# Kernel optimization log

Hardware: AMD Instinct MI355X
Metric: run time of the kernel (lower is better)

Reference implementation:

```python
import jax, jax.numpy as jnp
import numpy as np

N, FIN, F, H = 4096, 128, 64, 8
NEG = -1e10


def setup_inputs() -> dict:
    key = jax.random.key(0)
    ks = jax.random.split(key, 6)
    X = jax.random.normal(ks[0], (N, FIN), dtype=jnp.float32)
    # sparse-ish binary adjacency with self loops, stored dense (as the layer expects)
    A = (jax.random.uniform(ks[1], (N, N)) < 0.05).astype(jnp.int32)
    A = A.at[jnp.arange(N), jnp.arange(N)].set(1)
    W = jax.random.normal(ks[2], (H, FIN, F), dtype=jnp.float32) * (1.0 / np.sqrt(FIN))
    b = jnp.zeros((H, F), dtype=jnp.float32)
    a_self = jax.random.normal(ks[3], (H, F), dtype=jnp.float32) * (1.0 / np.sqrt(F))
    a_neigh = jax.random.normal(ks[4], (H, F), dtype=jnp.float32) * (1.0 / np.sqrt(F))
    return {"X": X, "A": A, "W": W, "b": b, "a_self": a_self, "a_neigh": a_neigh}


def reference(X, A, W, b, a_self, a_neigh):
    # Dropout layers run in inference mode in the original call -> identity.
    feats = jnp.einsum('nf,hfo->hno', X, W)              # [H, N, F]
    s_self = jnp.einsum('hno,ho->hn', feats, a_self)     # [H, N]
    s_neigh = jnp.einsum('hno,ho->hn', feats, a_neigh)   # [H, N]
    scores = s_self[:, :, None] + s_neigh[:, None, :]    # [H, N, N]
    scores = jnp.where(scores > 0, scores, 0.2 * scores)  # LeakyReLU(0.2)
    mask = (1.0 - A.astype(jnp.float32)) * NEG            # [N, N]
    attn = jax.nn.softmax(scores + mask[None], axis=-1)   # [H, N, N]
    out = jnp.einsum('hnm,hmo->hno', attn, feats) + b[:, None, :]
    out = jax.nn.elu(out)                                 # [H, N, F]
    # concat heads -> [N, H*F]
    return jnp.transpose(out, (1, 0, 2)).reshape(N, H * F)
```

## Files before the change

### kernel.cpp

```cpp
#include <hip/hip_runtime.h>
#include <cmath>


#define NN 4096
#define FIN 128
#define FF 64
#define HH 8

typedef _Float16 h2 __attribute__((ext_vector_type(2)));
typedef _Float16 h4 __attribute__((ext_vector_type(4)));
typedef _Float16 h8 __attribute__((ext_vector_type(8)));
typedef float f32x2 __attribute__((ext_vector_type(2)));
typedef float f32x4 __attribute__((ext_vector_type(4)));

union H8 {
  h8 v;
  h2 p[4];
};
union H4 {
  h4 v;
  h2 p[2];
};

static __device__ __forceinline__ float dot2acc(h2 a, float c) {
#if __has_builtin(__builtin_amdgcn_fdot2)
  return __builtin_amdgcn_fdot2(a, (h2){(_Float16)1.f, (_Float16)1.f}, c,
                                false);
#else
  return c + (float)a[0] + (float)a[1];
#endif
}

__global__ __launch_bounds__(256) void pack_kernel(
    const int* __restrict__ A, const float* __restrict__ W,
    const float* __restrict__ X, unsigned long long* __restrict__ bits,
    _Float16* __restrict__ Wsw, _Float16* __restrict__ Xsw) {
  const int b = blockIdx.x;
  const int tid = threadIdx.x;
  const int wave = tid >> 6, lane = tid & 63;
  if (b < NN) {
    __shared__ int ldsT[4][4][256];
    const int* ar = A + (size_t)b * NN;
    int4 v[4];
#pragma unroll
    for (int it = 0; it < 4; ++it) {
      const int g = wave * 4 + it;
      v[it] = *(const int4*)(ar + g * 256 + lane * 4);
    }
#pragma unroll
    for (int it = 0; it < 4; ++it) *(int4*)&ldsT[wave][it][lane * 4] = v[it];
    unsigned long long* br = bits + ((size_t)b << 6);
#pragma unroll
    for (int it = 0; it < 4; ++it) {
      const int g = wave * 4 + it;
      int w0 = ldsT[wave][it][0 * 64 + lane];
      int w1 = ldsT[wave][it][1 * 64 + lane];
      int w2 = ldsT[wave][it][2 * 64 + lane];
      int w3 = ldsT[wave][it][3 * 64 + lane];
      unsigned long long m0 = __ballot(w0 != 0);
      unsigned long long m1 = __ballot(w1 != 0);
      unsigned long long m2 = __ballot(w2 != 0);
      unsigned long long m3 = __ballot(w3 != 0);
      if (lane == 0) {
        ulonglong2 p0 = {m0, m1}, p1 = {m2, m3};
        *(ulonglong2*)(br + g * 4 + 0) = p0;
        *(ulonglong2*)(br + g * 4 + 2) = p1;
      }
    }
  } else if (b < NN + 2) {
    const int h0 = (b - NN) * 4;
    for (int h = h0; h < h0 + 4; ++h) {
      for (int c = tid; c < 1024; c += 256) {
        int ln = c & 63, nb = (c >> 6) & 3, kt = c >> 8;
        int f = nb * 16 + (ln & 15);
        int k0 = kt * 32 + (ln >> 4) * 8;
        h8 v;
#pragma unroll
        for (int j = 0; j < 8; ++j)
          v[j] = (_Float16)W[((size_t)(h * FIN) + k0 + j) * FF + f];
        *(h8*)(Wsw + ((size_t)(((h * 4 + kt) * 4 + nb) * 64 + ln)) * 8) = v;
      }
    }
  } else {
    const int tile = (b - NN - 2) * 4 + wave;
    const int l16 = lane & 15, quad = lane >> 4;
    const float* xr = X + (size_t)(tile * 16 + l16) * FIN;
#pragma unroll
    for (int kt = 0; kt < 4; ++kt) {
      int k0 = kt * 32 + quad * 8;
      f32x4 x0 = *(const f32x4*)(xr + k0);
      f32x4 x1 = *(const f32x4*)(xr + k0 + 4);
      h8 v = {(_Float16)x0[0], (_Float16)x0[1], (_Float16)x0[2],
              (_Float16)x0[3], (_Float16)x1[0], (_Float16)x1[1],
              (_Float16)x1[2], (_Float16)x1[3]};
      *(h8*)(Xsw + ((size_t)((tile * 4 + kt) * 64 + lane)) * 8) = v;
    }
  }
}

__global__ __launch_bounds__(256) void feats_kernel(
    const _Float16* __restrict__ Xsw, const _Float16* __restrict__ Wsw,
    const float* __restrict__ a_self, const float* __restrict__ a_neigh,
    _Float16* __restrict__ feats_sw, _Float16* __restrict__ es_h,
    _Float16* __restrict__ esn_h, _Float16* __restrict__ et_h,
    _Float16* __restrict__ etn_h) {
  const int h = blockIdx.y;
  const int tid = threadIdx.x, wave = tid >> 6, lane = tid & 63;
  const int l16 = lane & 15, quad = lane >> 4;
  const int rt = blockIdx.x * 4 + wave;
  const int r0 = rt * 16;

  f32x4 acc[4];
#pragma unroll
  for (int nb = 0; nb < 4; ++nb) acc[nb] = (f32x4){0.f, 0.f, 0.f, 0.f};

  const _Float16* xp = Xsw + ((size_t)(rt * 4) * 64 + lane) * 8;
  const _Float16* wp = Wsw + ((size_t)(h * 16) * 64 + lane) * 8;
  h8 Af[4];
#pragma unroll
  for (int kt = 0; kt < 4; ++kt) Af[kt] = *(const h8*)(xp + kt * 512);
#pragma unroll
  for (int kt = 0; kt < 4; ++kt)
#pragma unroll
    for (int nb = 0; nb < 4; ++nb) {
      h8 Bf = *(const h8*)(wp + (kt * 4 + nb) * 512);
      acc[nb] = __builtin_amdgcn_mfma_f32_16x16x32_f16(Af[kt], Bf, acc[nb], 0, 0, 0);
    }

  float as[4], an[4];
#pragma unroll
  for (int nb = 0; nb < 4; ++nb) {
    as[nb] = a_self[h * FF + nb * 16 + l16];
    an[nb] = a_neigh[h * FF + nb * 16 + l16];
  }
#pragma unroll
  for (int r = 0; r < 4; ++r) {
    float ps = acc[0][r] * as[0] + acc[1][r] * as[1] + acc[2][r] * as[2] +
               acc[3][r] * as[3];
    float pn = acc[0][r] * an[0] + acc[1][r] * an[1] + acc[2][r] * an[2] +
               acc[3][r] * an[3];
#pragma unroll
    for (int m = 1; m <= 8; m <<= 1) {
      ps += __shfl_xor(ps, m, 64);
      pn += __shfl_xor(pn, m, 64);
    }
    if (l16 == 0) {
      int node = h * NN + r0 + quad * 4 + r;
      es_h[node] = (_Float16)__expf(ps - 2.0f);
      esn_h[node] = (_Float16)__expf(0.2f * ps - 2.0f);
      et_h[node] = (_Float16)__expf(pn - 2.0f);
      etn_h[node] = (_Float16)__expf(0.2f * pn - 2.0f);
    }
  }

  const int kb = r0 >> 5;
  const int quadA = ((r0 >> 4) & 1) * 2 + (quad >> 1);
  const int jbase = (quad & 1) << 2;
#pragma unroll
  for (int nb = 0; nb < 4; ++nb) {
    h4 v = {(_Float16)acc[nb][0], (_Float16)acc[nb][1], (_Float16)acc[nb][2],
            (_Float16)acc[nb][3]};
    size_t off = ((size_t)((h * 128 + kb) * 4 + nb) << 9) +
                 ((quadA * 16 + l16) << 3) + jbase;
    *(h4*)(feats_sw + off) = v;
  }
}

__global__ __launch_bounds__(512, 4) void attn_kernel(
    const unsigned long long* __restrict__ Abits,
    const _Float16* __restrict__ feats_sw, const _Float16* __restrict__ es_h,
    const _Float16* __restrict__ esn_h, const _Float16* __restrict__ et_h,
    const _Float16* __restrict__ etn_h, const float* __restrict__ bias,
    float* __restrict__ out) {
  const int bid = blockIdx.x;
  const int h = bid & 7, n0 = (bid >> 3) << 6;
  const int tid = threadIdx.x, wave = tid >> 6, lane = tid & 63;
  const int l16 = lane & 15, quad = lane >> 4;

  __shared__ h4 lut16[16];
  __shared__ float accL[8][16][66];
  __shared__ float denL[8][64];
  if (tid < 16) {
    h4 m;
#pragma unroll
    for (int j = 0; j < 4; ++j) m[j] = (_Float16)((tid >> j) & 1);
    lut16[tid] = m;
  }
  __syncthreads();

  h2 esp[4], esnp[4];
#pragma unroll
  for (int rg = 0; rg < 4; ++rg) {
    _Float16 e = es_h[h * NN + n0 + rg * 16 + l16];
    _Float16 en = esn_h[h * NN + n0 + rg * 16 + l16];
    esp[rg] = (h2){e, e};
    esnp[rg] = (h2){en, en};
  }

  f32x4 acc[4][4];
  float dsA[4] = {0.f, 0.f, 0.f, 0.f}, dsB[4] = {0.f, 0.f, 0.f, 0.f};
#pragma unroll
  for (int rg = 0; rg < 4; ++rg)
#pragma unroll
    for (int nb = 0; nb < 4; ++nb) acc[rg][nb] = (f32x4){0.f, 0.f, 0.f, 0.f};

  const uint2* ab = (const uint2*)Abits;
  const int rowbase = n0 + l16;
  const _Float16* etp = et_h + h * NN + (quad << 3);
  const _Float16* etnp = etn_h + h * NN + (quad << 3);
  const _Float16* fb = feats_sw + ((size_t)h << 18) + (lane << 3);

  for (int ct = wave; ct < 64; ct += 8) {
    uint2 bits[4];
#pragma unroll
    for (int rg = 0; rg < 4; ++rg)
      bits[rg] = ab[((rowbase + rg * 16) << 6) + ct];
    const _Float16* fbt = fb + (ct << 12);
#pragma unroll
    for (int kf = 0; kf < 2; ++kf) {
      H8 ET, ETN;
      ET.v = *(const h8*)(etp + (ct << 6) + kf * 32);
      ETN.v = *(const h8*)(etnp + (ct << 6) + kf * 32);
      const _Float16* fk = fbt + (kf << 11);
      h8 B0 = *(const h8*)(fk);
      h8 B1 = *(const h8*)(fk + 512);
      h8 B2 = *(const h8*)(fk + 1024);
      h8 B3 = *(const h8*)(fk + 1536);
#pragma unroll
      for (int rg = 0; rg < 4; ++rg) {
        unsigned word = kf ? bits[rg].y : bits[rg].x;
        unsigned byt = (word >> (quad << 3)) & 0xFFu;
        H4 mlo, mhi;
        mlo.v = lut16[byt & 15u];
        mhi.v = lut16[byt >> 4];
        H8 P;
#pragma unroll
        for (int p = 0; p < 4; ++p) {
          h2 a = esp[rg] * ET.p[p];
          h2 b = esnp[rg] * ETN.p[p];
          h2 r = __builtin_elementwise_max(a, b);
          h2 pm = r * (p < 2 ? mlo.p[p] : mhi.p[p - 2]);
          P.p[p] = pm;
          if (p & 1)
            dsB[rg] = dot2acc(pm, dsB[rg]);
          else
            dsA[rg] = dot2acc(pm, dsA[rg]);
        }
        acc[rg][0] =
            __builtin_amdgcn_mfma_f32_16x16x32_f16(P.v, B0, acc[rg][0], 0, 0, 0);
        acc[rg][1] =
            __builtin_amdgcn_mfma_f32_16x16x32_f16(P.v, B1, acc[rg][1], 0, 0, 0);
        acc[rg][2] =
            __builtin_amdgcn_mfma_f32_16x16x32_f16(P.v, B2, acc[rg][2], 0, 0, 0);
        acc[rg][3] =
            __builtin_amdgcn_mfma_f32_16x16x32_f16(P.v, B3, acc[rg][3], 0, 0, 0);
      }
    }
  }

#pragma unroll
  for (int rg = 0; rg < 4; ++rg) {
    float d = dsA[rg] + dsB[rg];
    d += __shfl_xor(d, 16, 64);
    d += __shfl_xor(d, 32, 64);
    if (quad == 0) denL[wave][rg * 16 + l16] = d;
  }

  const int erow = tid >> 5, ec0 = (tid & 31) << 1;
#pragma unroll
  for (int ph = 0; ph < 4; ++ph) {
    __syncthreads();
#pragma unroll
    for (int nb = 0; nb < 4; ++nb)
#pragma unroll
      for (int r = 0; r < 4; ++r)
        accL[wave][quad * 4 + r][nb * 16 + l16] = acc[ph][nb][r];
    __syncthreads();
    const int grow = ph * 16 + erow;
    float dn = 0.f;
#pragma unroll
    for (int w = 0; w < 8; ++w) dn += denL[w][grow];
    float inv = 1.0f / dn;
    f32x2 v = (f32x2){0.f, 0.f};
#pragma unroll
    for (int w = 0; w < 8; ++w) v += *(const f32x2*)&accL[w][erow][ec0];
    const f32x2 bv = *(const f32x2*)(bias + h * FF + ec0);
#pragma unroll
    for (int i = 0; i < 2; ++i) {
      float x = v[i] * inv + bv[i];
      v[i] = x > 0.f ? x : (__expf(x) - 1.0f);
    }
    *(f32x2*)(out + (size_t)(n0 + grow) * (HH * FF) + h * FF + ec0) = v;
  }
}

extern "C" void kernel_launch(void* const* d_in, const int* in_sizes, int n_in,
                              void* d_out, int out_size, void* d_ws,
                              size_t ws_size, hipStream_t stream) {
  const float* X = (const float*)d_in[0];
  const int* A = (const int*)d_in[1];
  const float* W = (const float*)d_in[2];
  const float* b = (const float*)d_in[3];
  const float* a_self = (const float*)d_in[4];
  const float* a_neigh = (const float*)d_in[5];
  float* out = (float*)d_out;

  char* ws = (char*)d_ws;
  unsigned long long* Abits = (unsigned long long*)ws;
  _Float16* feats_sw = (_Float16*)(ws + (2u << 20));
  _Float16* es_h = (_Float16*)(ws + (6u << 20));
  _Float16* esn_h = (_Float16*)(ws + (6u << 20) + (64u << 10));
  _Float16* et_h = (_Float16*)(ws + (6u << 20) + (128u << 10));
  _Float16* etn_h = (_Float16*)(ws + (6u << 20) + (192u << 10));
  _Float16* Wsw = (_Float16*)(ws + (6u << 20) + (256u << 10));
  _Float16* Xsw = (_Float16*)(ws + (6u << 20) + (384u << 10));

  pack_kernel<<<NN + 66, 256, 0, stream>>>(A, W, X, Abits, Wsw, Xsw);
  feats_kernel<<<dim3(64, 8), 256, 0, stream>>>(Xsw, Wsw, a_self, a_neigh,
                                                feats_sw, es_h, esn_h, et_h,
                                                etn_h);
  attn_kernel<<<512, 512, 0, stream>>>(Abits, feats_sw, es_h, esn_h, et_h,
                                       etn_h, b, out);
}
```

Measured before the change: 148.3 us.

## Halve attention block size and software-pipeline adjacency and feature loads

The attention kernel now runs 256 threads (4 waves) per block instead of 512, so each wave covers 16 column tiles instead of 8. The main loop is software-pipelined: the next tile's adjacency bits, feature fragments and exponent vectors are prefetched into registers while the current half-tile's MFMAs run. The epilogue reduction is adjusted to 4 waves and uses 16-byte stores. This aims to hide global-load latency behind compute, at the cost of more register pressure and fewer waves per block to hide latency.

```diff
diff --git a/kernel.cpp b/kernel.cpp
--- a/kernel.cpp
+++ b/kernel.cpp
@@ -166,7 +166,7 @@
   }
 }
 
-__global__ __launch_bounds__(512, 4) void attn_kernel(
+__global__ __launch_bounds__(256, 3) void attn_kernel(
     const unsigned long long* __restrict__ Abits,
     const _Float16* __restrict__ feats_sw, const _Float16* __restrict__ es_h,
     const _Float16* __restrict__ esn_h, const _Float16* __restrict__ et_h,
@@ -178,8 +178,8 @@
   const int l16 = lane & 15, quad = lane >> 4;
 
   __shared__ h4 lut16[16];
-  __shared__ float accL[8][16][66];
-  __shared__ float denL[8][64];
+  __shared__ float accL[4][16][66];
+  __shared__ float denL[4][64];
   if (tid < 16) {
     h4 m;
 #pragma unroll
@@ -205,58 +205,101 @@
     for (int nb = 0; nb < 4; ++nb) acc[rg][nb] = (f32x4){0.f, 0.f, 0.f, 0.f};
 
   const uint2* ab = (const uint2*)Abits;
-  const int rowbase = n0 + l16;
+  int bOff[4];
+#pragma unroll
+  for (int rg = 0; rg < 4; ++rg) bOff[rg] = (n0 + rg * 16 + l16) << 6;
   const _Float16* etp = et_h + h * NN + (quad << 3);
   const _Float16* etnp = etn_h + h * NN + (quad << 3);
   const _Float16* fb = feats_sw + ((size_t)h << 18) + (lane << 3);
 
-  for (int ct = wave; ct < 64; ct += 8) {
-    uint2 bits[4];
-#pragma unroll
-    for (int rg = 0; rg < 4; ++rg)
-      bits[rg] = ab[((rowbase + rg * 16) << 6) + ct];
-    const _Float16* fbt = fb + (ct << 12);
-#pragma unroll
-    for (int kf = 0; kf < 2; ++kf) {
-      H8 ET, ETN;
-      ET.v = *(const h8*)(etp + (ct << 6) + kf * 32);
-      ETN.v = *(const h8*)(etnp + (ct << 6) + kf * 32);
-      const _Float16* fk = fbt + (kf << 11);
-      h8 B0 = *(const h8*)(fk);
-      h8 B1 = *(const h8*)(fk + 512);
-      h8 B2 = *(const h8*)(fk + 1024);
-      h8 B3 = *(const h8*)(fk + 1536);
-#pragma unroll
-      for (int rg = 0; rg < 4; ++rg) {
-        unsigned word = kf ? bits[rg].y : bits[rg].x;
-        unsigned byt = (word >> (quad << 3)) & 0xFFu;
-        H4 mlo, mhi;
-        mlo.v = lut16[byt & 15u];
-        mhi.v = lut16[byt >> 4];
-        H8 P;
-#pragma unroll
-        for (int p = 0; p < 4; ++p) {
-          h2 a = esp[rg] * ET.p[p];
-          h2 b = esnp[rg] * ETN.p[p];
-          h2 r = __builtin_elementwise_max(a, b);
-          h2 pm = r * (p < 2 ? mlo.p[p] : mhi.p[p - 2]);
-          P.p[p] = pm;
-          if (p & 1)
-            dsB[rg] = dot2acc(pm, dsB[rg]);
-          else
-            dsA[rg] = dot2acc(pm, dsA[rg]);
-        }
-        acc[rg][0] =
-            __builtin_amdgcn_mfma_f32_16x16x32_f16(P.v, B0, acc[rg][0], 0, 0, 0);
-        acc[rg][1] =
-            __builtin_amdgcn_mfma_f32_16x16x32_f16(P.v, B1, acc[rg][1], 0, 0, 0);
-        acc[rg][2] =
-            __builtin_amdgcn_mfma_f32_16x16x32_f16(P.v, B2, acc[rg][2], 0, 0, 0);
-        acc[rg][3] =
-            __builtin_amdgcn_mfma_f32_16x16x32_f16(P.v, B3, acc[rg][3], 0, 0, 0);
-      }
-    }
-  }
+#define COMPUTE_KF(w0_, w1_, w2_, w3_, Bq0, Bq1, Bq2, Bq3, ETu, ETNu)         \
+  do {                                                                        \
+    const unsigned wl_[4] = {w0_, w1_, w2_, w3_};                             \
+    _Pragma("unroll") for (int rg = 0; rg < 4; ++rg) {                        \
+      const unsigned byt_ = (wl_[rg] >> (quad << 3)) & 0xFFu;                 \
+      H4 mlo_, mhi_;                                                          \
+      mlo_.v = lut16[byt_ & 15u];                                             \
+      mhi_.v = lut16[byt_ >> 4];                                              \
+      H8 P_;                                                                  \
+      _Pragma("unroll") for (int p = 0; p < 4; ++p) {                         \
+        h2 a_ = esp[rg] * ETu.p[p];                                           \
+        h2 b_ = esnp[rg] * ETNu.p[p];                                         \
+        h2 r_ = __builtin_elementwise_max(a_, b_);                            \
+        h2 pm_ = r_ * (p < 2 ? mlo_.p[p] : mhi_.p[p - 2]);                    \
+        P_.p[p] = pm_;                                                        \
+        if (p & 1)                                                            \
+          dsB[rg] = dot2acc(pm_, dsB[rg]);                                    \
+        else                                                                  \
+          dsA[rg] = dot2acc(pm_, dsA[rg]);                                    \
+      }                                                                       \
+      acc[rg][0] = __builtin_amdgcn_mfma_f32_16x16x32_f16(P_.v, Bq0,          \
+                                                          acc[rg][0], 0, 0,   \
+                                                          0);                 \
+      acc[rg][1] = __builtin_amdgcn_mfma_f32_16x16x32_f16(P_.v, Bq1,          \
+                                                          acc[rg][1], 0, 0,   \
+                                                          0);                 \
+      acc[rg][2] = __builtin_amdgcn_mfma_f32_16x16x32_f16(P_.v, Bq2,          \
+                                                          acc[rg][2], 0, 0,   \
+                                                          0);                 \
+      acc[rg][3] = __builtin_amdgcn_mfma_f32_16x16x32_f16(P_.v, Bq3,          \
+                                                          acc[rg][3], 0, 0,   \
+                                                          0);                 \
+    }                                                                         \
+  } while (0)
+
+  int ct = wave;
+  uint2 bitsC[4], bitsN[4];
+#pragma unroll
+  for (int rg = 0; rg < 4; ++rg) bitsC[rg] = ab[bOff[rg] + ct];
+  H8 ET0, ET1, ETN0, ETN1;
+  ET0.v = *(const h8*)(etp + (ct << 6));
+  ET1.v = *(const h8*)(etp + (ct << 6) + 32);
+  ETN0.v = *(const h8*)(etnp + (ct << 6));
+  ETN1.v = *(const h8*)(etnp + (ct << 6) + 32);
+  h8 BA0, BA1, BA2, BA3, BB0, BB1, BB2, BB3;
+  {
+    const _Float16* f0 = fb + ((size_t)ct << 12);
+    BA0 = *(const h8*)(f0);
+    BA1 = *(const h8*)(f0 + 512);
+    BA2 = *(const h8*)(f0 + 1024);
+    BA3 = *(const h8*)(f0 + 1536);
+  }
+
+  for (int it = 0; it < 16; ++it) {
+    const int ctn = (ct + 4) & 63;
+    {
+      const _Float16* f1 = fb + ((size_t)ct << 12) + 2048;
+      BB0 = *(const h8*)(f1);
+      BB1 = *(const h8*)(f1 + 512);
+      BB2 = *(const h8*)(f1 + 1024);
+      BB3 = *(const h8*)(f1 + 1536);
+    }
+#pragma unroll
+    for (int rg = 0; rg < 4; ++rg) bitsN[rg] = ab[bOff[rg] + ctn];
+
+    COMPUTE_KF(bitsC[0].x, bitsC[1].x, bitsC[2].x, bitsC[3].x, BA0, BA1, BA2,
+               BA3, ET0, ETN0);
+
+    ET0.v = *(const h8*)(etp + (ctn << 6));
+    ETN0.v = *(const h8*)(etnp + (ctn << 6));
+    {
+      const _Float16* f0n = fb + ((size_t)ctn << 12);
+      BA0 = *(const h8*)(f0n);
+      BA1 = *(const h8*)(f0n + 512);
+      BA2 = *(const h8*)(f0n + 1024);
+      BA3 = *(const h8*)(f0n + 1536);
+    }
+
+    COMPUTE_KF(bitsC[0].y, bitsC[1].y, bitsC[2].y, bitsC[3].y, BB0, BB1, BB2,
+               BB3, ET1, ETN1);
+
+    ET1.v = *(const h8*)(etp + (ctn << 6) + 32);
+    ETN1.v = *(const h8*)(etnp + (ctn << 6) + 32);
+#pragma unroll
+    for (int rg = 0; rg < 4; ++rg) bitsC[rg] = bitsN[rg];
+    ct = ctn;
+  }
+#undef COMPUTE_KF
 
 #pragma unroll
   for (int rg = 0; rg < 4; ++rg) {
@@ -266,7 +309,7 @@
     if (quad == 0) denL[wave][rg * 16 + l16] = d;
   }
 
-  const int erow = tid >> 5, ec0 = (tid & 31) << 1;
+  const int erow = tid >> 4, ec0 = (tid & 15) << 2;
 #pragma unroll
   for (int ph = 0; ph < 4; ++ph) {
     __syncthreads();
@@ -277,20 +320,26 @@
         accL[wave][quad * 4 + r][nb * 16 + l16] = acc[ph][nb][r];
     __syncthreads();
     const int grow = ph * 16 + erow;
-    float dn = 0.f;
-#pragma unroll
-    for (int w = 0; w < 8; ++w) dn += denL[w][grow];
+    float dn = denL[0][grow] + denL[1][grow] + denL[2][grow] + denL[3][grow];
     float inv = 1.0f / dn;
-    f32x2 v = (f32x2){0.f, 0.f};
-#pragma unroll
-    for (int w = 0; w < 8; ++w) v += *(const f32x2*)&accL[w][erow][ec0];
-    const f32x2 bv = *(const f32x2*)(bias + h * FF + ec0);
-#pragma unroll
-    for (int i = 0; i < 2; ++i) {
-      float x = v[i] * inv + bv[i];
-      v[i] = x > 0.f ? x : (__expf(x) - 1.0f);
-    }
-    *(f32x2*)(out + (size_t)(n0 + grow) * (HH * FF) + h * FF + ec0) = v;
+    f32x2 v0 = (f32x2){0.f, 0.f}, v1 = (f32x2){0.f, 0.f};
+#pragma unroll
+    for (int w = 0; w < 4; ++w) {
+      v0 += *(const f32x2*)&accL[w][erow][ec0];
+      v1 += *(const f32x2*)&accL[w][erow][ec0 + 2];
+    }
+    const f32x4 bv = *(const f32x4*)(bias + h * FF + ec0);
+    f32x4 o;
+    o[0] = v0[0];
+    o[1] = v0[1];
+    o[2] = v1[0];
+    o[3] = v1[1];
+#pragma unroll
+    for (int i = 0; i < 4; ++i) {
+      float x = o[i] * inv + bv[i];
+      o[i] = x > 0.f ? x : (__expf(x) - 1.0f);
+    }
+    *(f32x4*)(out + (size_t)(n0 + grow) * (HH * FF) + h * FF + ec0) = o;
   }
 }
 
@@ -319,6 +368,6 @@
   feats_kernel<<<dim3(64, 8), 256, 0, stream>>>(Xsw, Wsw, a_self, a_neigh,
                                                 feats_sw, es_h, esn_h, et_h,
                                                 etn_h);
-  attn_kernel<<<512, 512, 0, stream>>>(Abits, feats_sw, es_h, esn_h, et_h,
+  attn_kernel<<<512, 256, 0, stream>>>(Abits, feats_sw, es_h, esn_h, et_h,
                                        etn_h, b, out);
 }
```

After: 150.9 us. No clear change (+1.7%).

## Restructure attention kernel with LDS triple-buffered async staging and per-wave row split

Applied to the files above, without the earlier changes.

The attention kernel now gives each block 128 rows. Each wave owns 16 rows and walks all key columns, instead of splitting columns across waves and reducing the partial sums through LDS. Feature, et and mask-bit tiles are staged into a three-deep LDS ring with global_load_lds and explicit vmcnt waits. This overlaps memory traffic with the MFMA work and removes the cross-wave accumulator reduction. The LUT-based mask expansion is replaced by a bitfield-extract and perm AND mask. In exchange, the grid has half as many blocks and occupancy is lower, and the hand-written waitcnt counts are fragile.

```diff
diff --git a/kernel.cpp b/kernel.cpp
--- a/kernel.cpp
+++ b/kernel.cpp
@@ -17,9 +17,9 @@
   h8 v;
   h2 p[4];
 };
-union H4 {
-  h4 v;
-  h2 p[2];
+union U2 {
+  h2 h;
+  unsigned u;
 };
 
 static __device__ __forceinline__ float dot2acc(h2 a, float c) {
@@ -29,6 +29,24 @@
 #else
   return c + (float)a[0] + (float)a[1];
 #endif
+}
+
+static __device__ __forceinline__ unsigned mask2(unsigned w, int j) {
+#if __has_builtin(__builtin_amdgcn_sbfe) && __has_builtin(__builtin_amdgcn_perm)
+  int lo = __builtin_amdgcn_sbfe((int)w, j, 1);
+  int hi = __builtin_amdgcn_sbfe((int)w, j + 1, 1);
+  return __builtin_amdgcn_perm((unsigned)hi, (unsigned)lo, 0x05040100u);
+#else
+  int lo = ((int)(w << (31 - j))) >> 31;
+  int hi = ((int)(w << (30 - j))) >> 31;
+  return ((unsigned)lo & 0xFFFFu) | ((unsigned)hi << 16);
+#endif
+}
+
+static __device__ __forceinline__ void gload16(const void* g, void* l) {
+  __builtin_amdgcn_global_load_lds(
+      (const __attribute__((address_space(1))) unsigned int*)g,
+      (__attribute__((address_space(3))) unsigned int*)l, 16, 0, 0);
 }
 
 __global__ __launch_bounds__(256) void pack_kernel(
@@ -166,131 +184,133 @@
   }
 }
 
-__global__ __launch_bounds__(512, 4) void attn_kernel(
+__global__ __launch_bounds__(512, 2) void attn_kernel(
     const unsigned long long* __restrict__ Abits,
     const _Float16* __restrict__ feats_sw, const _Float16* __restrict__ es_h,
     const _Float16* __restrict__ esn_h, const _Float16* __restrict__ et_h,
     const _Float16* __restrict__ etn_h, const float* __restrict__ bias,
     float* __restrict__ out) {
   const int bid = blockIdx.x;
-  const int h = bid & 7, n0 = (bid >> 3) << 6;
+  const int h = bid & 7, n0 = (bid >> 3) << 7;
   const int tid = threadIdx.x, wave = tid >> 6, lane = tid & 63;
   const int l16 = lane & 15, quad = lane >> 4;
-
-  __shared__ h4 lut16[16];
-  __shared__ float accL[8][16][66];
-  __shared__ float denL[8][64];
-  if (tid < 16) {
-    h4 m;
-#pragma unroll
-    for (int j = 0; j < 4; ++j) m[j] = (_Float16)((tid >> j) & 1);
-    lut16[tid] = m;
-  }
-  __syncthreads();
-
-  h2 esp[4], esnp[4];
-#pragma unroll
-  for (int rg = 0; rg < 4; ++rg) {
-    _Float16 e = es_h[h * NN + n0 + rg * 16 + l16];
-    _Float16 en = esn_h[h * NN + n0 + rg * 16 + l16];
-    esp[rg] = (h2){e, e};
-    esnp[rg] = (h2){en, en};
-  }
-
-  f32x4 acc[4][4];
-  float dsA[4] = {0.f, 0.f, 0.f, 0.f}, dsB[4] = {0.f, 0.f, 0.f, 0.f};
-#pragma unroll
-  for (int rg = 0; rg < 4; ++rg)
-#pragma unroll
-    for (int nb = 0; nb < 4; ++nb) acc[rg][nb] = (f32x4){0.f, 0.f, 0.f, 0.f};
-
-  const uint2* ab = (const uint2*)Abits;
-  const int rowbase = n0 + l16;
-  const _Float16* etp = et_h + h * NN + (quad << 3);
-  const _Float16* etnp = etn_h + h * NN + (quad << 3);
-  const _Float16* fb = feats_sw + ((size_t)h << 18) + (lane << 3);
-
-  for (int ct = wave; ct < 64; ct += 8) {
-    uint2 bits[4];
-#pragma unroll
-    for (int rg = 0; rg < 4; ++rg)
-      bits[rg] = ab[((rowbase + rg * 16) << 6) + ct];
-    const _Float16* fbt = fb + (ct << 12);
-#pragma unroll
-    for (int kf = 0; kf < 2; ++kf) {
-      H8 ET, ETN;
-      ET.v = *(const h8*)(etp + (ct << 6) + kf * 32);
-      ETN.v = *(const h8*)(etnp + (ct << 6) + kf * 32);
-      const _Float16* fk = fbt + (kf << 11);
-      h8 B0 = *(const h8*)(fk);
-      h8 B1 = *(const h8*)(fk + 512);
-      h8 B2 = *(const h8*)(fk + 1024);
-      h8 B3 = *(const h8*)(fk + 1536);
-#pragma unroll
-      for (int rg = 0; rg < 4; ++rg) {
-        unsigned word = kf ? bits[rg].y : bits[rg].x;
-        unsigned byt = (word >> (quad << 3)) & 0xFFu;
-        H4 mlo, mhi;
-        mlo.v = lut16[byt & 15u];
-        mhi.v = lut16[byt >> 4];
+  const int shq = quad << 3;
+
+  __shared__ __align__(16) char smem[3 * 20480];
+
+  const int myrow = n0 + (wave << 4) + l16;
+  _Float16 e = es_h[h * NN + myrow];
+  _Float16 en = esn_h[h * NN + myrow];
+  const h2 esp = (h2){e, e};
+  const h2 esnp = (h2){en, en};
+
+  f32x4 acc[4];
+#pragma unroll
+  for (int nb = 0; nb < 4; ++nb) acc[nb] = (f32x4){0.f, 0.f, 0.f, 0.f};
+  float dsA = 0.f, dsB = 0.f;
+
+  const char* gF = (const char*)feats_sw + ((size_t)h << 19);
+  const char* gE = (const char*)et_h + (h << 13);
+  const char* gEN = (const char*)etn_h + (h << 13);
+  const char* gB = (const char*)Abits + ((size_t)n0 << 9);
+
+#define STAGE(s_, bw_)                                                        \
+  do {                                                                        \
+    char* L_ = smem + (bw_)*20480;                                            \
+    const char* src_ = gF + ((size_t)(s_) << 14) + (wave << 11) + (lane << 4);\
+    gload16(src_, L_ + (wave << 11) + (lane << 4));                           \
+    gload16(src_ + 1024, L_ + (wave << 11) + 1024 + (lane << 4));             \
+    if (wave == 0)                                                            \
+      gload16(gE + ((s_) << 8) + (l16 << 4), L_ + 16384 + (lane << 4));       \
+    if (wave == 1)                                                            \
+      gload16(gEN + ((s_) << 8) + (l16 << 4), L_ + 17408 + (lane << 4));      \
+    if (wave == 2)                                                            \
+      gload16(gB + ((size_t)lane << 9) + ((s_) << 4),                         \
+              L_ + 18432 + (lane << 4));                                      \
+    if (wave == 3)                                                            \
+      gload16(gB + ((size_t)(64 + lane) << 9) + ((s_) << 4),                  \
+              L_ + 18432 + 1024 + (lane << 4));                               \
+  } while (0)
+
+  STAGE(0, 0);
+  STAGE(1, 1);
+
+  for (int s = 0; s < 32; ++s) {
+    const int bC = s % 3;
+    if (s < 30) {
+      STAGE(s + 2, (s + 2) % 3);
+      __builtin_amdgcn_sched_barrier(0);
+      if (wave < 4)
+        asm volatile("s_waitcnt vmcnt(6)" ::: "memory");
+      else
+        asm volatile("s_waitcnt vmcnt(4)" ::: "memory");
+    } else if (s == 30) {
+      __builtin_amdgcn_sched_barrier(0);
+      if (wave < 4)
+        asm volatile("s_waitcnt vmcnt(3)" ::: "memory");
+      else
+        asm volatile("s_waitcnt vmcnt(2)" ::: "memory");
+    } else {
+      __builtin_amdgcn_sched_barrier(0);
+      asm volatile("s_waitcnt vmcnt(0)" ::: "memory");
+    }
+    __builtin_amdgcn_sched_barrier(0);
+    __builtin_amdgcn_s_barrier();
+
+    const char* L = smem + bC * 20480;
+#pragma unroll
+    for (int c = 0; c < 2; ++c) {
+      unsigned long long myb = *(const unsigned long long*)(
+          L + 18432 + (((wave << 4) + l16) << 4) + (c << 3));
+#pragma unroll
+      for (int kf = 0; kf < 2; ++kf) {
+        H8 ET, ETN;
+        ET.v = *(const h8*)(L + 16384 + (c << 7) + (kf << 6) + (quad << 4));
+        ETN.v = *(const h8*)(L + 17408 + (c << 7) + (kf << 6) + (quad << 4));
+        const char* fB = L + (c << 13) + (kf << 12) + (lane << 4);
+        h8 B0 = *(const h8*)(fB);
+        h8 B1 = *(const h8*)(fB + 1024);
+        h8 B2 = *(const h8*)(fB + 2048);
+        h8 B3 = *(const h8*)(fB + 3072);
+        unsigned wsw = (unsigned)(myb >> (kf ? 32 : 0)) >> shq;
         H8 P;
 #pragma unroll
         for (int p = 0; p < 4; ++p) {
-          h2 a = esp[rg] * ET.p[p];
-          h2 b = esnp[rg] * ETN.p[p];
-          h2 r = __builtin_elementwise_max(a, b);
-          h2 pm = r * (p < 2 ? mlo.p[p] : mhi.p[p - 2]);
-          P.p[p] = pm;
+          h2 a_ = esp * ET.p[p];
+          h2 b_ = esnp * ETN.p[p];
+          h2 r_ = __builtin_elementwise_max(a_, b_);
+          U2 u_;
+          u_.h = r_;
+          u_.u &= mask2(wsw, 2 * p);
+          P.p[p] = u_.h;
           if (p & 1)
-            dsB[rg] = dot2acc(pm, dsB[rg]);
+            dsB = dot2acc(u_.h, dsB);
           else
-            dsA[rg] = dot2acc(pm, dsA[rg]);
+            dsA = dot2acc(u_.h, dsA);
         }
-        acc[rg][0] =
-            __builtin_amdgcn_mfma_f32_16x16x32_f16(P.v, B0, acc[rg][0], 0, 0, 0);
-        acc[rg][1] =
-            __builtin_amdgcn_mfma_f32_16x16x32_f16(P.v, B1, acc[rg][1], 0, 0, 0);
-        acc[rg][2] =
-            __builtin_amdgcn_mfma_f32_16x16x32_f16(P.v, B2, acc[rg][2], 0, 0, 0);
-        acc[rg][3] =
-            __builtin_amdgcn_mfma_f32_16x16x32_f16(P.v, B3, acc[rg][3], 0, 0, 0);
+        acc[0] = __builtin_amdgcn_mfma_f32_16x16x32_f16(P.v, B0, acc[0], 0, 0, 0);
+        acc[1] = __builtin_amdgcn_mfma_f32_16x16x32_f16(P.v, B1, acc[1], 0, 0, 0);
+        acc[2] = __builtin_amdgcn_mfma_f32_16x16x32_f16(P.v, B2, acc[2], 0, 0, 0);
+        acc[3] = __builtin_amdgcn_mfma_f32_16x16x32_f16(P.v, B3, acc[3], 0, 0, 0);
       }
     }
   }
-
-#pragma unroll
-  for (int rg = 0; rg < 4; ++rg) {
-    float d = dsA[rg] + dsB[rg];
-    d += __shfl_xor(d, 16, 64);
-    d += __shfl_xor(d, 32, 64);
-    if (quad == 0) denL[wave][rg * 16 + l16] = d;
-  }
-
-  const int erow = tid >> 5, ec0 = (tid & 31) << 1;
-#pragma unroll
-  for (int ph = 0; ph < 4; ++ph) {
-    __syncthreads();
-#pragma unroll
-    for (int nb = 0; nb < 4; ++nb)
-#pragma unroll
-      for (int r = 0; r < 4; ++r)
-        accL[wave][quad * 4 + r][nb * 16 + l16] = acc[ph][nb][r];
-    __syncthreads();
-    const int grow = ph * 16 + erow;
-    float dn = 0.f;
-#pragma unroll
-    for (int w = 0; w < 8; ++w) dn += denL[w][grow];
-    float inv = 1.0f / dn;
-    f32x2 v = (f32x2){0.f, 0.f};
-#pragma unroll
-    for (int w = 0; w < 8; ++w) v += *(const f32x2*)&accL[w][erow][ec0];
-    const f32x2 bv = *(const f32x2*)(bias + h * FF + ec0);
-#pragma unroll
-    for (int i = 0; i < 2; ++i) {
-      float x = v[i] * inv + bv[i];
-      v[i] = x > 0.f ? x : (__expf(x) - 1.0f);
-    }
-    *(f32x2*)(out + (size_t)(n0 + grow) * (HH * FF) + h * FF + ec0) = v;
+#undef STAGE
+
+  float den = dsA + dsB;
+  den += __shfl_xor(den, 16, 64);
+  den += __shfl_xor(den, 32, 64);
+  const int orow = n0 + (wave << 4) + (quad << 2);
+#pragma unroll
+  for (int r = 0; r < 4; ++r) {
+    float dr = __shfl(den, (quad << 2) + r, 64);
+    float inv = 1.0f / dr;
+#pragma unroll
+    for (int nb = 0; nb < 4; ++nb) {
+      float x = acc[nb][r] * inv + bias[h * FF + nb * 16 + l16];
+      x = x > 0.f ? x : (__expf(x) - 1.0f);
+      out[(size_t)(orow + r) * (HH * FF) + h * FF + nb * 16 + l16] = x;
+    }
   }
 }
 
@@ -319,6 +339,6 @@
   feats_kernel<<<dim3(64, 8), 256, 0, stream>>>(Xsw, Wsw, a_self, a_neigh,
                                                 feats_sw, es_h, esn_h, et_h,
                                                 etn_h);
-  attn_kernel<<<512, 512, 0, stream>>>(Abits, feats_sw, es_h, esn_h, et_h,
+  attn_kernel<<<256, 512, 0, stream>>>(Abits, feats_sw, es_h, esn_h, et_h,
                                        etn_h, b, out);
 }
```

Result: no change. 146.0 us (-1.6%).
